# Kernel optimization log

Measured on AMD Instinct MI355X. Metric: run time of the kernel, lower is better.

## Reference

```python
import jax, jax.numpy as jnp
import numpy as np

B, S, D = 2, 2048, 1024
H, KS = 16, 64

def setup_inputs() -> dict:
    key = jax.random.key(0)
    k1, k2, k3, k4, k5 = jax.random.split(key, 5)
    return {
        "x": jax.random.normal(k1, (B, S, D), dtype=jnp.float32),
        "Wq": jax.random.normal(k2, (D, KS, H), dtype=jnp.float32) * 0.02,
        "Wk": jax.random.normal(k3, (D, KS, H), dtype=jnp.float32) * 0.02,
        "Wv": jax.random.normal(k4, (D, KS, H), dtype=jnp.float32) * 0.02,
        "kernel": jax.random.normal(k5, (H * KS, KS), dtype=jnp.float32) * 0.02,
    }

def reference(x, Wq, Wk, Wv, kernel):
    b, s, d = x.shape
    ks, h = Wq.shape[1], Wq.shape[2]
    # projections: heads-last layout [b, s, ks, h]
    q = jnp.einsum('bsd,dkh->bskh', x, Wq)
    k = jnp.einsum('bsd,dkh->bskh', x, Wk)
    v = jnp.einsum('bsd,dkh->bskh', x, Wv)
    # scores [b, i(query), l(key), h]
    scores = jnp.einsum('bikh,blkh->bilh', q, k) / jnp.sqrt(jnp.float32(ks))
    # strictly-upper-triangular (future) mask, as in the original:
    # band_part(ones,0,-1) - eye  ->  1 where l > i
    li = jnp.arange(s)
    mask = (li[None, :] > li[:, None]).astype(jnp.float32)  # [s, s]
    scores = scores - 1e8 * mask[None, :, :, None]
    weights = jax.nn.softmax(scores, axis=2)  # softmax over key axis l
    heads = jnp.einsum('bilh,blkh->bikh', weights, v)  # [b, s, ks, h]
    heads = heads.reshape(b, s, ks * h)  # row-major flatten of (ks, h), matching tf.reshape
    return heads @ kernel  # [b, s, ks]
```

## Files before the change

### kernel.cpp

```cpp
#include <hip/hip_runtime.h>
#include <hip/hip_bf16.h>

#define BB 2
#define SS 2048
#define DD 1024
#define HH 16
#define KSZ 64

typedef __attribute__((ext_vector_type(8))) short s16x8;
typedef __attribute__((ext_vector_type(4))) short s16x4;
typedef __attribute__((ext_vector_type(4))) float f32x4;
typedef __attribute__((ext_vector_type(8))) unsigned short u16x8;
typedef __attribute__((ext_vector_type(4))) unsigned short u16x4;
typedef __attribute__((ext_vector_type(2))) unsigned int u32x2;
typedef unsigned short u16;

__device__ __forceinline__ u16 bf16rne(float f) {
  unsigned int u = __float_as_uint(f);
  unsigned int r = (u + 0x7FFFu + ((u >> 16) & 1u)) >> 16;
  return (u16)r;
}

__device__ __forceinline__ unsigned int cvtpk_bf16(float lo, float hi) {
  unsigned int r;
  asm("v_cvt_pk_bf16_f32 %0, %1, %2" : "=v"(r) : "v"(lo), "v"(hi));
  return r;
}

#if __has_builtin(__builtin_amdgcn_mfma_f32_16x16x16_bf16)
__device__ __forceinline__ f32x4 mfma16(s16x4 a, s16x4 b, f32x4 c) {
  return __builtin_amdgcn_mfma_f32_16x16x16_bf16(a, b, c, 0, 0, 0);
}
#elif __has_builtin(__builtin_amdgcn_mfma_f32_16x16x16bf16_1k)
__device__ __forceinline__ f32x4 mfma16(s16x4 a, s16x4 b, f32x4 c) {
  return __builtin_amdgcn_mfma_f32_16x16x16bf16_1k(a, b, c, 0, 0, 0);
}
#else
__device__ __forceinline__ f32x4 mfma16(s16x4 a, s16x4 b, f32x4 c) {
  asm("s_nop 1\n\tv_mfma_f32_16x16x16_bf16 %0, %1, %2, %0"
      : "+v"(c) : "v"(a), "v"(b));
  return c;
}
#endif

__device__ __forceinline__ void lds_dma16(const u16* g, u16* l) {
  __builtin_amdgcn_global_load_lds(
      (const __attribute__((address_space(1))) unsigned int*)(const void*)g,
      (__attribute__((address_space(3))) unsigned int*)(void*)l, 16, 0, 0);
}

__global__ __launch_bounds__(256) void prep_all(
    const float* __restrict__ x, const float* __restrict__ Wq,
    const float* __restrict__ Wk, const float* __restrict__ Wv,
    const float* __restrict__ kern, u16* __restrict__ xb,
    u16* __restrict__ Wt, u16* __restrict__ BpT) {
  __shared__ float Ts[64][65];
  const int bid = blockIdx.x;
  const int tid = threadIdx.x;
  if (bid < 2048) {
    int idx = (bid * 256 + tid) * 8;
    float4 a = *(const float4*)(x + idx);
    float4 b = *(const float4*)(x + idx + 4);
    u16x8 v;
    v[0] = bf16rne(a.x); v[1] = bf16rne(a.y); v[2] = bf16rne(a.z); v[3] = bf16rne(a.w);
    v[4] = bf16rne(b.x); v[5] = bf16rne(b.y); v[6] = bf16rne(b.z); v[7] = bf16rne(b.w);
    *(u16x8*)(xb + idx) = v;
  } else if (bid < 2816) {
    const int bx = bid - 2048;
    const int p = bx >> 8, rem = bx & 255;
    const int d0 = (rem & 15) * 64, n0 = (rem >> 4) * 64;
    const float* W = (p == 0) ? Wq : (p == 1) ? Wk : Wv;
    u16* Wo = Wt + (size_t)p * DD * DD;
    #pragma unroll
    for (int i = 0; i < 4; ++i) {
      int f4 = tid + i * 256;
      int r = f4 >> 4, c4 = f4 & 15;
      float4 v = *(const float4*)(W + (size_t)(d0 + r) * DD + n0 + c4 * 4);
      Ts[r][c4 * 4 + 0] = v.x; Ts[r][c4 * 4 + 1] = v.y;
      Ts[r][c4 * 4 + 2] = v.z; Ts[r][c4 * 4 + 3] = v.w;
    }
    __syncthreads();
    #pragma unroll
    for (int i = 0; i < 4; ++i) {
      int ch = tid + i * 256;
      int n = ch >> 4, d4 = ch & 15;
      u16x4 o;
      #pragma unroll
      for (int j = 0; j < 4; ++j) o[j] = bf16rne(Ts[d4 * 4 + j][n]);
      *(u16x4*)(Wo + (size_t)(n0 + n) * DD + d0 + d4 * 4) = o;
    }
  } else {
    const int n = bid - 2816;
    const int k4 = tid * 4;
    u16x4 o;
    #pragma unroll
    for (int j = 0; j < 4; ++j) {
      int kp = k4 + j;
      int h = kp >> 6, k = kp & 63;
      o[j] = bf16rne(kern[(size_t)(k * HH + h) * KSZ + n]);
    }
    *(u16x4*)(BpT + (size_t)n * (HH * KSZ) + k4) = o;
  }
}

__global__ __launch_bounds__(512, 2) void proj_kernel(
    const u16* __restrict__ xb, const u16* __restrict__ Wt,
    u16* __restrict__ qkvT) {
  const int bid = blockIdx.x;
  const int p   = bid >> 6;
  const int rem = bid & 63;
  const int mt  = rem & 15, nt = rem >> 4;
  const int m0 = mt * 256, n0 = nt * 256;
  const u16* W = Wt + (size_t)p * DD * DD;
  u16* outp = qkvT + (size_t)p * (BB * HH * SS * KSZ);

  __shared__ __align__(16) unsigned char raw[98304];
  u16* lds = (u16*)raw;
  u16* Cs  = (u16*)raw;

  const int tid = threadIdx.x;
  const int wave = tid >> 6, lane = tid & 63;
  const int g = lane >> 4, c = lane & 15;
  const int mbase = (wave & 1) * 128, nbase = (wave >> 1) * 64;

  const int lr = lane >> 2, lc = lane & 3;
  const int swz = (lc ^ ((lr >> 1) & 3)) * 8;
  const int rA0 = wave * 32, rA1 = wave * 32 + 16;
  const u16* srcA0 = xb + (size_t)(m0 + rA0 + lr) * DD + swz;
  const u16* srcA1 = xb + (size_t)(m0 + rA1 + lr) * DD + swz;
  const u16* srcB0 = W  + (size_t)(n0 + rA0 + lr) * DD + swz;
  const u16* srcB1 = W  + (size_t)(n0 + rA1 + lr) * DD + swz;
  const int sl0 = rA0 * 32, sl1 = rA1 * 32;

  f32x4 acc[8][4];
  #pragma unroll
  for (int i = 0; i < 8; ++i)
    #pragma unroll
    for (int j = 0; j < 4; ++j) acc[i][j] = {0.f, 0.f, 0.f, 0.f};

  {
    u16* A0 = lds;                 u16* B0 = lds + 8192;
    u16* A1 = lds + 16384;         u16* B1 = lds + 16384 + 8192;
    lds_dma16(srcA0, A0 + sl0);       lds_dma16(srcA1, A0 + sl1);
    lds_dma16(srcB0, B0 + sl0);       lds_dma16(srcB1, B0 + sl1);
    lds_dma16(srcA0 + 32, A1 + sl0);  lds_dma16(srcA1 + 32, A1 + sl1);
    lds_dma16(srcB0 + 32, B1 + sl0);  lds_dma16(srcB1 + 32, B1 + sl1);
  }

  const int jsw = (c >> 1) & 3;
  int cr = 0;
  #pragma unroll 1
  for (int t = 0; t < 31; ++t) {
    asm volatile("s_waitcnt vmcnt(4)" ::: "memory");
    __builtin_amdgcn_s_barrier();
    __builtin_amdgcn_sched_barrier(0);
    if (t <= 29) {
      const int st = cr ? cr - 1 : 2;
      const int ko = (t + 2) * 32;
      u16* An = lds + st * 16384;
      u16* Bn = An + 8192;
      lds_dma16(srcA0 + ko, An + sl0);  lds_dma16(srcA1 + ko, An + sl1);
      lds_dma16(srcB0 + ko, Bn + sl0);  lds_dma16(srcB1 + ko, Bn + sl1);
    }
    u16* Ac = lds + cr * 16384;
    u16* Bc = Ac + 8192;
    s16x8 af[8], bfr[4];
    #pragma unroll
    for (int mf = 0; mf < 8; ++mf)
      af[mf] = *(const s16x8*)&Ac[(mbase + mf * 16 + c) * 32 + ((g ^ jsw) * 8)];
    #pragma unroll
    for (int nf = 0; nf < 4; ++nf)
      bfr[nf] = *(const s16x8*)&Bc[(nbase + nf * 16 + c) * 32 + ((g ^ jsw) * 8)];
    #pragma unroll
    for (int mf = 0; mf < 8; ++mf)
      #pragma unroll
      for (int nf = 0; nf < 4; ++nf)
        acc[mf][nf] = __builtin_amdgcn_mfma_f32_16x16x32_bf16(
            af[mf], bfr[nf], acc[mf][nf], 0, 0, 0);
    cr = (cr >= 2) ? 0 : cr + 1;
  }
  asm volatile("s_waitcnt vmcnt(0)" ::: "memory");
  __builtin_amdgcn_s_barrier();
  __builtin_amdgcn_sched_barrier(0);
  {
    u16* Ac = lds + cr * 16384;
    u16* Bc = Ac + 8192;
    s16x8 af[8], bfr[4];
    #pragma unroll
    for (int mf = 0; mf < 8; ++mf)
      af[mf] = *(const s16x8*)&Ac[(mbase + mf * 16 + c) * 32 + ((g ^ jsw) * 8)];
    #pragma unroll
    for (int nf = 0; nf < 4; ++nf)
      bfr[nf] = *(const s16x8*)&Bc[(nbase + nf * 16 + c) * 32 + ((g ^ jsw) * 8)];
    #pragma unroll
    for (int mf = 0; mf < 8; ++mf)
      #pragma unroll
      for (int nf = 0; nf < 4; ++nf)
        acc[mf][nf] = __builtin_amdgcn_mfma_f32_16x16x32_bf16(
            af[mf], bfr[nf], acc[mf][nf], 0, 0, 0);
  }

  const float cscale = (p == 0) ? 0.125f * 1.44269504f : 1.0f;
  #pragma unroll 1
  for (int hhalf = 0; hhalf < 2; ++hhalf) {
    __syncthreads();
    if ((wave & 1) == hhalf) {
      #pragma unroll
      for (int mf = 0; mf < 8; ++mf)
        #pragma unroll
        for (int nf = 0; nf < 4; ++nf)
          #pragma unroll
          for (int r = 0; r < 4; ++r)
            Cs[(mf * 16 + g * 4 + r) * 264 + nbase + nf * 16 + c] =
                bf16rne(acc[mf][nf][r] * cscale);
    }
    __syncthreads();
    const int rowg = m0 + hhalf * 128;
    const int bb = rowg >> 11;
    if (p < 2) {
      #pragma unroll
      for (int i = 0; i < 8; ++i) {
        int idx = tid + i * 512;
        int hh = idx & 15, kq = (idx >> 4) & 1, row = idx >> 5;
        int s = (rowg + row) & 2047;
        u16x8 v;
        #pragma unroll
        for (int j = 0; j < 8; ++j) v[j] = Cs[row * 264 + (kq * 8 + j) * 16 + hh];
        *(u16x8*)(outp + ((size_t)(bb * HH + hh) * SS + s) * KSZ +
                  (n0 >> 4) + kq * 8) = v;
      }
    } else {
      const int s0 = rowg & 2047;
      #pragma unroll
      for (int i = 0; i < 8; ++i) {
        int idx = tid + i * 512;
        int col = idx & 255, s8 = idx >> 8;
        int hh = col & 15, kk = col >> 4;
        u16x8 v;
        #pragma unroll
        for (int j = 0; j < 8; ++j) v[j] = Cs[(s8 * 8 + j) * 264 + col];
        *(u16x8*)(outp + ((size_t)(bb * HH + hh) * KSZ + (n0 >> 4) + kk) * SS +
                  s0 + s8 * 8) = v;
      }
    }
  }
}

__global__ __launch_bounds__(256, 2) void attn_kernel(
    const u16* __restrict__ qkvT, u16* __restrict__ headsB) {
  const int bid = blockIdx.x;
  const int hb = bid & 31;
  const int q5 = bid >> 5;
  const int qt = (q5 < 8) ? q5 : 23 - q5;
  const int h = hb & 15, b = hb >> 4;
  const size_t plane = (size_t)(b * HH + h) * SS * KSZ;
  const size_t PSZ = (size_t)BB * HH * SS * KSZ;
  const u16* Qg = qkvT + plane;
  const u16* Kg = qkvT + PSZ + plane;
  const u16* Vg = qkvT + 2 * PSZ + plane;

  __shared__ u16 Ks[2][64 * 64];
  __shared__ u16 Vt[2][64 * 64];

  const int tid = threadIdx.x;
  const int lane = tid & 63;
  const int g = lane >> 4, c = lane & 15;
  const int wq0 = (tid >> 6) * 32;
  const int sr = tid >> 3, sc = tid & 7;
  const int soA = sr * 64 + ((sc ^ (sr & 7)) * 8);
  const int soB = soA + 32 * 64;

  const int nt = 2 * qt + 2;

  s16x8 bq[2][2];
  #pragma unroll
  for (int sq = 0; sq < 2; ++sq) {
    const size_t qrow = (size_t)(qt * 128 + wq0 + sq * 16 + c) * KSZ;
    bq[sq][0] = *(const s16x8*)(Qg + qrow + g * 8);
    bq[sq][1] = *(const s16x8*)(Qg + qrow + 32 + g * 8);
  }

  u16x8 kr0 = *(const u16x8*)(Kg + (size_t)sr * KSZ + sc * 8);
  u16x8 kr1 = *(const u16x8*)(Kg + (size_t)(sr + 32) * KSZ + sc * 8);
  u16x8 vr0 = *(const u16x8*)(Vg + (size_t)sr * SS + sc * 8);
  u16x8 vr1 = *(const u16x8*)(Vg + (size_t)(sr + 32) * SS + sc * 8);
  *(u16x8*)&Ks[0][soA] = kr0; *(u16x8*)&Ks[0][soB] = kr1;
  *(u16x8*)&Vt[0][soA] = vr0; *(u16x8*)&Vt[0][soB] = vr1;
  kr0 = *(const u16x8*)(Kg + (size_t)(64 + sr) * KSZ + sc * 8);
  kr1 = *(const u16x8*)(Kg + (size_t)(64 + sr + 32) * KSZ + sc * 8);
  vr0 = *(const u16x8*)(Vg + (size_t)sr * SS + 64 + sc * 8);
  vr1 = *(const u16x8*)(Vg + (size_t)(sr + 32) * SS + 64 + sc * 8);
  __syncthreads();

  f32x4 o[2][4];
  #pragma unroll
  for (int sq = 0; sq < 2; ++sq)
    #pragma unroll
    for (int mf = 0; mf < 4; ++mf) o[sq][mf] = {0.f, 0.f, 0.f, 0.f};
  float l_i[2] = {0.f, 0.f};
  const int cswz = c & 7;

  #pragma unroll 1
  for (int t = 0; t < nt; ++t) {
    const int buf = t & 1;
    if (t + 1 < nt) {
      const int nb = buf ^ 1;
      *(u16x8*)&Ks[nb][soA] = kr0; *(u16x8*)&Ks[nb][soB] = kr1;
      *(u16x8*)&Vt[nb][soA] = vr0; *(u16x8*)&Vt[nb][soB] = vr1;
      if (t + 2 < nt) {
        const int kv2 = t + 2;
        kr0 = *(const u16x8*)(Kg + (size_t)(kv2 * 64 + sr) * KSZ + sc * 8);
        kr1 = *(const u16x8*)(Kg + (size_t)(kv2 * 64 + sr + 32) * KSZ + sc * 8);
        vr0 = *(const u16x8*)(Vg + (size_t)sr * SS + kv2 * 64 + sc * 8);
        vr1 = *(const u16x8*)(Vg + (size_t)(sr + 32) * SS + kv2 * 64 + sc * 8);
      }
    }
    f32x4 s[2][4];
    #pragma unroll
    for (int sq = 0; sq < 2; ++sq)
      #pragma unroll
      for (int mf = 0; mf < 4; ++mf) s[sq][mf] = {0.f, 0.f, 0.f, 0.f};
    __builtin_amdgcn_s_setprio(1);
    #pragma unroll
    for (int ks = 0; ks < 2; ++ks) {
      #pragma unroll
      for (int mf = 0; mf < 4; ++mf) {
        s16x8 ak = *(const s16x8*)&Ks[buf][(mf * 16 + c) * 64 +
                                          (((ks * 4 + g) ^ cswz) * 8)];
        s[0][mf] = __builtin_amdgcn_mfma_f32_16x16x32_bf16(ak, bq[0][ks],
                                                           s[0][mf], 0, 0, 0);
        s[1][mf] = __builtin_amdgcn_mfma_f32_16x16x32_bf16(ak, bq[1][ks],
                                                           s[1][mf], 0, 0, 0);
      }
    }
    __builtin_amdgcn_s_setprio(0);
    if (t >= 2 * qt) {
      const int rel = (t - 2 * qt) * 64;
      #pragma unroll
      for (int sq = 0; sq < 2; ++sq) {
        const int qloc = wq0 + sq * 16 + c;
        #pragma unroll
        for (int mf = 0; mf < 4; ++mf)
          #pragma unroll
          for (int r = 0; r < 4; ++r)
            if (rel + mf * 16 + g * 4 + r > qloc) s[sq][mf][r] = -1e30f;
      }
    }
    s16x4 bp[2][4];
    #pragma unroll
    for (int sq = 0; sq < 2; ++sq) {
      #pragma unroll
      for (int mf = 0; mf < 4; ++mf) {
        float p0 = __builtin_amdgcn_exp2f(s[sq][mf][0]);
        float p1 = __builtin_amdgcn_exp2f(s[sq][mf][1]);
        float p2 = __builtin_amdgcn_exp2f(s[sq][mf][2]);
        float p3 = __builtin_amdgcn_exp2f(s[sq][mf][3]);
        l_i[sq] += (p0 + p1) + (p2 + p3);
        u32x2 pk;
        pk[0] = cvtpk_bf16(p0, p1);
        pk[1] = cvtpk_bf16(p2, p3);
        bp[sq][mf] = __builtin_bit_cast(s16x4, pk);
      }
    }
    __builtin_amdgcn_s_setprio(1);
    #pragma unroll
    for (int mf = 0; mf < 4; ++mf) {
      #pragma unroll
      for (int kb = 0; kb < 4; ++kb) {
        s16x4 av = *(const s16x4*)&Vt[buf][(mf * 16 + c) * 64 +
                                           (((kb * 2 + (g >> 1)) ^ cswz) * 8) +
                                           (g & 1) * 4];
        o[0][mf] = mfma16(av, bp[0][kb], o[0][mf]);
        o[1][mf] = mfma16(av, bp[1][kb], o[1][mf]);
      }
    }
    __builtin_amdgcn_s_setprio(0);
    __syncthreads();
  }
  #pragma unroll
  for (int sq = 0; sq < 2; ++sq) {
    float l = l_i[sq];
    l += __shfl_xor(l, 16);
    l += __shfl_xor(l, 32);
    const float inv = 1.0f / l;
    const int q = qt * 128 + wq0 + sq * 16 + c;
    #pragma unroll
    for (int mf = 0; mf < 4; ++mf) {
      u16x4 hv;
      #pragma unroll
      for (int r = 0; r < 4; ++r) hv[r] = bf16rne(o[sq][mf][r] * inv);
      *(u16x4*)(headsB + plane + (size_t)q * KSZ + mf * 16 + g * 4) = hv;
    }
  }
}

__global__ __launch_bounds__(256) void out_kernel(
    const u16* __restrict__ headsB, const u16* __restrict__ BpT,
    float* __restrict__ out) {
  const int m0 = blockIdx.x * 16;
  const int tid = threadIdx.x;
  const int wave = tid >> 6, lane = tid & 63;
  const int g = lane >> 4, c = lane & 15;

  const int m = m0 + c;
  const int b = m >> 11, s = m & 2047;

  f32x4 acc[4];
  #pragma unroll
  for (int nf = 0; nf < 4; ++nf) acc[nf] = {0.f, 0.f, 0.f, 0.f};

  #pragma unroll
  for (int it = 0; it < 8; ++it) {
    const int kb = wave * 256 + it * 32;
    const int hh = kb >> 6, kk = (kb & 63) + g * 8;
    s16x8 a = *(const s16x8*)(headsB +
        ((size_t)(b * HH + hh) * SS + s) * KSZ + kk);
    #pragma unroll
    for (int nf = 0; nf < 4; ++nf) {
      s16x8 bf = *(const s16x8*)(BpT +
          (size_t)(nf * 16 + c) * (HH * KSZ) + kb + g * 8);
      acc[nf] = __builtin_amdgcn_mfma_f32_16x16x32_bf16(a, bf, acc[nf], 0, 0, 0);
    }
  }

  __shared__ __align__(16) float red[4][64][16];
  #pragma unroll
  for (int nf = 0; nf < 4; ++nf)
    *(f32x4*)&red[wave][lane][nf * 4] = acc[nf];
  __syncthreads();

  const int mi = tid >> 4, n4 = (tid & 15) * 4;
  const int gg = mi >> 2, rr = mi & 3;
  float4 res;
  float* rp = &res.x;
  #pragma unroll
  for (int j = 0; j < 4; ++j) {
    int n = n4 + j;
    int cc = n & 15, nf = n >> 4;
    rp[j] = red[0][gg * 16 + cc][nf * 4 + rr] + red[1][gg * 16 + cc][nf * 4 + rr] +
            red[2][gg * 16 + cc][nf * 4 + rr] + red[3][gg * 16 + cc][nf * 4 + rr];
  }
  *(float4*)(out + (size_t)(m0 + mi) * KSZ + n4) = res;
}

extern "C" void kernel_launch(void* const* d_in, const int* in_sizes, int n_in,
                              void* d_out, int out_size, void* d_ws, size_t ws_size,
                              hipStream_t stream) {
  const float* x    = (const float*)d_in[0];
  const float* Wq   = (const float*)d_in[1];
  const float* Wk   = (const float*)d_in[2];
  const float* Wv   = (const float*)d_in[3];
  const float* kern = (const float*)d_in[4];
  float* out = (float*)d_out;

  u16* xb     = (u16*)d_ws;
  u16* Wt     = xb + (size_t)4096 * 1024;
  u16* qkvT   = Wt + (size_t)3 * 1024 * 1024;
  u16* headsB = qkvT + (size_t)3 * BB * HH * SS * KSZ;
  u16* BpT    = headsB + (size_t)BB * HH * SS * KSZ;

  prep_all<<<dim3(2880), 256, 0, stream>>>(x, Wq, Wk, Wv, kern, xb, Wt, BpT);
  proj_kernel<<<dim3(192), 512, 0, stream>>>(xb, Wt, qkvT);
  attn_kernel<<<dim3(512), 256, 0, stream>>>(qkvT, headsB);
  out_kernel<<<dim3(256), 256, 0, stream>>>(headsB, BpT, out);
}
```

Before: 161.4 us.

## Restructure projection GEMM main loop into 4-phase ping-pong with interleaved DMA

Replaces the 3-stage K=32 LDS ring in the projection GEMM with a double-buffered K=64 tile. Each tile is split into four phases that interleave LDS fragment reads, async global-to-LDS loads for the next tile, and MFMA bursts run with raised wave priority. The aim is to overlap memory traffic with matrix math and cut per-iteration barrier overhead. LDS use rises to 128KB per block, which may reduce occupancy below the launch-bounds target of 2 blocks, and there are more barriers per tile.

```diff
diff --git a/kernel.cpp b/kernel.cpp
--- a/kernel.cpp
+++ b/kernel.cpp
@@ -114,7 +114,7 @@
   const u16* W = Wt + (size_t)p * DD * DD;
   u16* outp = qkvT + (size_t)p * (BB * HH * SS * KSZ);
 
-  __shared__ __align__(16) unsigned char raw[98304];
+  __shared__ __align__(16) unsigned char raw[131072];
   u16* lds = (u16*)raw;
   u16* Cs  = (u16*)raw;
 
@@ -138,66 +138,67 @@
     #pragma unroll
     for (int j = 0; j < 4; ++j) acc[i][j] = {0.f, 0.f, 0.f, 0.f};
 
-  {
-    u16* A0 = lds;                 u16* B0 = lds + 8192;
-    u16* A1 = lds + 16384;         u16* B1 = lds + 16384 + 8192;
-    lds_dma16(srcA0, A0 + sl0);       lds_dma16(srcA1, A0 + sl1);
-    lds_dma16(srcB0, B0 + sl0);       lds_dma16(srcB1, B0 + sl1);
-    lds_dma16(srcA0 + 32, A1 + sl0);  lds_dma16(srcA1 + 32, A1 + sl1);
-    lds_dma16(srcB0 + 32, B1 + sl0);  lds_dma16(srcB1 + 32, B1 + sl1);
-  }
+  lds_dma16(srcA0, lds + 0 + sl0);          lds_dma16(srcA1, lds + 0 + sl1);
+  lds_dma16(srcB0, lds + 16384 + sl0);      lds_dma16(srcB1, lds + 16384 + sl1);
+  lds_dma16(srcA0 + 32, lds + 8192 + sl0);  lds_dma16(srcA1 + 32, lds + 8192 + sl1);
+  lds_dma16(srcB0 + 32, lds + 24576 + sl0); lds_dma16(srcB1 + 32, lds + 24576 + sl1);
+  asm volatile("s_waitcnt vmcnt(4)" ::: "memory");
+  __builtin_amdgcn_s_barrier();
 
   const int jsw = (c >> 1) & 3;
-  int cr = 0;
   #pragma unroll 1
-  for (int t = 0; t < 31; ++t) {
-    asm volatile("s_waitcnt vmcnt(4)" ::: "memory");
-    __builtin_amdgcn_s_barrier();
-    __builtin_amdgcn_sched_barrier(0);
-    if (t <= 29) {
-      const int st = cr ? cr - 1 : 2;
-      const int ko = (t + 2) * 32;
-      u16* An = lds + st * 16384;
-      u16* Bn = An + 8192;
-      lds_dma16(srcA0 + ko, An + sl0);  lds_dma16(srcA1 + ko, An + sl1);
-      lds_dma16(srcB0 + ko, Bn + sl0);  lds_dma16(srcB1 + ko, Bn + sl1);
-    }
-    u16* Ac = lds + cr * 16384;
-    u16* Bc = Ac + 8192;
-    s16x8 af[8], bfr[4];
-    #pragma unroll
-    for (int mf = 0; mf < 8; ++mf)
-      af[mf] = *(const s16x8*)&Ac[(mbase + mf * 16 + c) * 32 + ((g ^ jsw) * 8)];
-    #pragma unroll
-    for (int nf = 0; nf < 4; ++nf)
-      bfr[nf] = *(const s16x8*)&Bc[(nbase + nf * 16 + c) * 32 + ((g ^ jsw) * 8)];
-    #pragma unroll
-    for (int mf = 0; mf < 8; ++mf)
-      #pragma unroll
-      for (int nf = 0; nf < 4; ++nf)
-        acc[mf][nf] = __builtin_amdgcn_mfma_f32_16x16x32_bf16(
-            af[mf], bfr[nf], acc[mf][nf], 0, 0, 0);
-    cr = (cr >= 2) ? 0 : cr + 1;
-  }
-  asm volatile("s_waitcnt vmcnt(0)" ::: "memory");
-  __builtin_amdgcn_s_barrier();
-  __builtin_amdgcn_sched_barrier(0);
-  {
-    u16* Ac = lds + cr * 16384;
-    u16* Bc = Ac + 8192;
-    s16x8 af[8], bfr[4];
-    #pragma unroll
-    for (int mf = 0; mf < 8; ++mf)
-      af[mf] = *(const s16x8*)&Ac[(mbase + mf * 16 + c) * 32 + ((g ^ jsw) * 8)];
-    #pragma unroll
-    for (int nf = 0; nf < 4; ++nf)
-      bfr[nf] = *(const s16x8*)&Bc[(nbase + nf * 16 + c) * 32 + ((g ^ jsw) * 8)];
-    #pragma unroll
-    for (int mf = 0; mf < 8; ++mf)
-      #pragma unroll
-      for (int nf = 0; nf < 4; ++nf)
-        acc[mf][nf] = __builtin_amdgcn_mfma_f32_16x16x32_bf16(
-            af[mf], bfr[nf], acc[mf][nf], 0, 0, 0);
+  for (int kt = 0; kt < 16; ++kt) {
+    const int cur = kt & 1;
+    u16* bufc = lds + cur * 32768;
+    u16* bufn = lds + (cur ^ 1) * 32768;
+    const bool last = (kt == 15);
+    const int knext = (kt + 1) * 64;
+    s16x8 bfr[4];
+    #pragma unroll
+    for (int ph = 0; ph < 4; ++ph) {
+      const int ks = ph >> 1, mh = ph & 1;
+      u16* Ap = bufc + ks * 8192;
+      u16* Bp = bufc + 16384 + ks * 8192;
+      s16x8 af[4];
+      #pragma unroll
+      for (int mf = 0; mf < 4; ++mf)
+        af[mf] = *(const s16x8*)&Ap[(mbase + mh * 64 + mf * 16 + c) * 32 +
+                                    ((g ^ jsw) * 8)];
+      if (mh == 0) {
+        #pragma unroll
+        for (int nf = 0; nf < 4; ++nf)
+          bfr[nf] = *(const s16x8*)&Bp[(nbase + nf * 16 + c) * 32 +
+                                       ((g ^ jsw) * 8)];
+      }
+      if (!last) {
+        if (ph == 0) { lds_dma16(srcA0 + knext, bufn + sl0);
+                       lds_dma16(srcA1 + knext, bufn + sl1); }
+        if (ph == 1) { lds_dma16(srcB0 + knext, bufn + 16384 + sl0);
+                       lds_dma16(srcB1 + knext, bufn + 16384 + sl1); }
+        if (ph == 2) { lds_dma16(srcA0 + knext + 32, bufn + 8192 + sl0);
+                       lds_dma16(srcA1 + knext + 32, bufn + 8192 + sl1); }
+        if (ph == 3) { lds_dma16(srcB0 + knext + 32, bufn + 24576 + sl0);
+                       lds_dma16(srcB1 + knext + 32, bufn + 24576 + sl1); }
+      }
+      __builtin_amdgcn_s_barrier();
+      asm volatile("s_waitcnt lgkmcnt(0)" ::: "memory");
+      __builtin_amdgcn_sched_barrier(0);
+      __builtin_amdgcn_s_setprio(1);
+      #pragma unroll
+      for (int mf = 0; mf < 4; ++mf)
+        #pragma unroll
+        for (int nf = 0; nf < 4; ++nf)
+          acc[mh * 4 + mf][nf] = __builtin_amdgcn_mfma_f32_16x16x32_bf16(
+              af[mf], bfr[nf], acc[mh * 4 + mf][nf], 0, 0, 0);
+      __builtin_amdgcn_s_setprio(0);
+      if (ph == 1) {
+        if (!last) asm volatile("s_waitcnt vmcnt(4)" ::: "memory");
+        else       asm volatile("s_waitcnt vmcnt(0)" ::: "memory");
+      }
+      if (ph == 3 && !last)
+        asm volatile("s_waitcnt vmcnt(4)" ::: "memory");
+      __builtin_amdgcn_s_barrier();
+    }
   }
 
   const float cscale = (p == 0) ? 0.125f * 1.44269504f : 1.0f;
```

Result: no change. 161.2 us (-0.1%).
